# Optimization experiments

Hardware: AMD Instinct MI355X
Metric: run time of the kernel (lower is better)

## Reference

```python
import jax, jax.numpy as jnp
import numpy as np

NEG_SLOPE = 0.01  # torch nn.LeakyReLU default


def setup_inputs() -> dict:
    key = jax.random.key(0)
    kq, kk, kv, km, kw = jax.random.split(key, 5)
    B, Lq, Lk, Dk, Dv = 4, 2048, 2048, 512, 512
    q = jax.random.normal(kq, (B, Lq, Dk), dtype=jnp.float32)
    k = jax.random.normal(kk, (B, Lk, Dk), dtype=jnp.float32)
    v = jax.random.normal(kv, (B, Lk, Dv), dtype=jnp.float32)
    attn_mask = jax.random.randint(km, (B, Lq, Lk), 0, 2).astype(jnp.int32)
    # xavier_normal for (Dk, 1): std = sqrt(2 / (Dk + 1))
    weight = jax.random.normal(kw, (Dk, 1), dtype=jnp.float32) * np.sqrt(2.0 / (Dk + 1))
    return {"q": q, "k": k, "v": v, "attn_mask": attn_mask, "weight": weight}


def reference(q, k, v, attn_mask, weight):
    # (q - k) @ w  ==  (q @ w) - (k @ w): avoid the [B,Lq,Lk,Dk] intermediate.
    qw = jnp.einsum('bqd,do->bq', q, weight)  # [B, Lq]
    kw = jnp.einsum('bkd,do->bk', k, weight)  # [B, Lk]
    scores = qw[:, :, None] - kw[:, None, :]  # [B, Lq, Lk]
    attn = jnp.where(scores >= 0, scores, NEG_SLOPE * scores)  # LeakyReLU
    masked = attn_mask == 0
    attn = jnp.where(masked, -jnp.inf, attn)
    attn = jax.nn.softmax(attn, axis=2)
    attn = jnp.where(masked, 0.0, attn)
    # dropout omitted (eval mode / identity for reference correctness)
    output = jnp.einsum('bqk,bkd->bqd', attn, v)  # bmm
    return output, attn
```

## Files before the change

### kernel.cpp

```cpp
#include <hip/hip_runtime.h>
#include <math.h>

#define BB 4
#define LQ 2048
#define LK 2048
#define DK 512
#define DV 512

typedef __attribute__((ext_vector_type(8))) _Float16 f16x8;
typedef __attribute__((ext_vector_type(2))) _Float16 f16x2;
typedef __attribute__((ext_vector_type(4))) float f32x4;

#define WS_QW    0
#define WS_KW    8192
#define WS_M     16384
#define WS_INV   24576
#define WS_VF16  32768
#define NOUT     ((size_t)BB * LQ * DV)

__device__ __forceinline__ unsigned int pk2(float a, float b) {
    auto h = __builtin_amdgcn_cvt_pkrtz(a, b);
    return __builtin_bit_cast(unsigned int, h);
}

__device__ __forceinline__ void lds_barrier() {
    __builtin_amdgcn_sched_barrier(0);
    asm volatile("s_waitcnt lgkmcnt(0)\n\ts_barrier" ::: "memory");
    __builtin_amdgcn_sched_barrier(0);
}

__global__ __launch_bounds__(256) void qkw_kernel(const float* __restrict__ q,
                                                  const float* __restrict__ k,
                                                  const float* __restrict__ w,
                                                  float* __restrict__ ws) {
    int gw   = (int)((blockIdx.x * blockDim.x + threadIdx.x) >> 6);
    int lane = threadIdx.x & 63;
    const int nq = BB * LQ;
    const float* row = (gw < nq) ? (q + (size_t)gw * DK) : (k + (size_t)(gw - nq) * DK);

    float acc = 0.f;
#pragma unroll
    for (int j = 0; j < DK; j += 256) {
        int idx = j + lane * 4;
        float4 rv = *reinterpret_cast<const float4*>(row + idx);
        float4 wv = *reinterpret_cast<const float4*>(w + idx);
        acc += rv.x * wv.x + rv.y * wv.y + rv.z * wv.z + rv.w * wv.w;
    }
#pragma unroll
    for (int off = 32; off >= 1; off >>= 1) acc += __shfl_xor(acc, off, 64);
    if (lane == 0) ws[gw] = acc;
}

__global__ __launch_bounds__(256) void vpack_kernel(const float* __restrict__ v,
                                                    unsigned short* __restrict__ vF) {
    __shared__ float tile[32][517];
    const int k32 = blockIdx.x;
    const int b   = blockIdx.y;
    const int k0  = k32 * 32;
    const int t   = threadIdx.x;

#pragma unroll
    for (int i = 0; i < 16; ++i) {
        int flat = i * 256 + t;
        int row  = flat >> 7;
        int c4   = flat & 127;
        float4 f = *reinterpret_cast<const float4*>(
            v + ((size_t)(b * LK + k0 + row)) * DV + c4 * 4);
        tile[row][c4 * 4 + 0] = f.x;
        tile[row][c4 * 4 + 1] = f.y;
        tile[row][c4 * 4 + 2] = f.z;
        tile[row][c4 * 4 + 3] = f.w;
    }
    __syncthreads();

    const int w = t >> 6, l = t & 63;
    const int rbase = (l >> 4) * 8;
#pragma unroll
    for (int f = 0; f < 8; ++f) {
        int n16 = w * 8 + f;
        int col = n16 * 16 + (l & 15);
        f16x8 vv;
#pragma unroll
        for (int j = 0; j < 8; ++j) vv[j] = (_Float16)tile[rbase + j][col];
        size_t u16base = (((size_t)(b * 32 + n16)) * 64 + k32) * 512;
        *reinterpret_cast<f16x8*>(vF + u16base + l * 8) = vv;
    }
}

__global__ __launch_bounds__(256) void rowstat_kernel(const int* __restrict__ mask,
                                                      float* __restrict__ ws,
                                                      float* __restrict__ attn) {
    __shared__ float kws[LK];
    const int b = (blockIdx.x * 4) / LQ;
    const int t = threadIdx.x;

    const float4* kw4 = reinterpret_cast<const float4*>(ws + WS_KW + b * LK);
#pragma unroll
    for (int i = 0; i < 2; ++i)
        reinterpret_cast<float4*>(kws)[t + i * 256] = kw4[t + i * 256];
    __syncthreads();

    const int wave = t >> 6, lane = t & 63;
    const int rid  = blockIdx.x * 4 + wave;
    const float qwv = ws[WS_QW + rid];
    const int* mrow = mask + (size_t)rid * LK;

    float m = -INFINITY, s = 0.f;
    unsigned int mybits = 0;
#pragma unroll
    for (int i = 0; i < 8; ++i) {
        int e = (i * 64 + lane) * 4;
        int4  mi = *reinterpret_cast<const int4*>(mrow + e);
        float4 kv = reinterpret_cast<const float4*>(kws)[i * 64 + lane];
        float vals[4] = {kv.x, kv.y, kv.z, kv.w};
        int   msks[4] = {mi.x, mi.y, mi.z, mi.w};

        unsigned int bits = (msks[0] ? 1u : 0u) | (msks[1] ? 2u : 0u) |
                            (msks[2] ? 4u : 0u) | (msks[3] ? 8u : 0u);
        mybits |= bits << (i * 4);

#pragma unroll
        for (int j = 0; j < 4; ++j) {
            float sc = qwv - vals[j];
            sc = fmaxf(sc, 0.01f * sc);
            if (msks[j]) {
                if (sc > m) { s = s * __expf(m - sc) + 1.f; m = sc; }
                else        { s += __expf(sc - m); }
            }
        }
    }
#pragma unroll
    for (int off = 32; off >= 1; off >>= 1) {
        float mo = __shfl_xor(m, off, 64);
        float so = __shfl_xor(s, off, 64);
        float M  = fmaxf(m, mo);
        float sa = (m  == M) ? s  : s  * __expf(m  - M);
        float sb = (mo == M) ? so : so * __expf(mo - M);
        m = M; s = sa + sb;
    }
    const float inv = (s > 0.f) ? 1.f / s : 0.f;
    if (lane == 0) {
        ws[WS_M   + rid] = m;
        ws[WS_INV + rid] = inv;
    }

    float* arow = attn + (size_t)rid * LK;
#pragma unroll
    for (int i = 0; i < 8; ++i) {
        float4 kv = reinterpret_cast<const float4*>(kws)[i * 64 + lane];
        float vals[4] = {kv.x, kv.y, kv.z, kv.w};
        unsigned int bits = (mybits >> (i * 4)) & 0xFu;
        float p[4];
#pragma unroll
        for (int j = 0; j < 4; ++j) {
            float sc = qwv - vals[j];
            sc = fmaxf(sc, 0.01f * sc);
            p[j] = (bits & (1u << j)) ? __expf(sc - m) * inv : 0.f;
        }
        *reinterpret_cast<float4*>(arow + (i * 64 + lane) * 4) =
            make_float4(p[0], p[1], p[2], p[3]);
    }
}

__global__ __launch_bounds__(256, 2) void pv_kernel(
        const float* __restrict__ attn,
        const unsigned short* __restrict__ vF,
        float* __restrict__ out) {
    __shared__ unsigned int pH32[2][2048];
    __shared__ unsigned int pL32[2][2048];

    const int bid  = blockIdx.x;
    const int xcd  = bid & 7;
    const int rest = bid >> 3;
    const int g    = rest >> 2;
    const int ns   = rest & 3;
    const int qt4b = g * 8 + xcd;
    const int b    = qt4b & 3;
    const int qt   = qt4b >> 2;
    const int ksteps = LK >> 6;

    const int t = threadIdx.x;
    const int w = t >> 6, l = t & 63;

    const int row_a = (t >> 6) * 16 + (t & 15);
    const int kb    = ((t >> 4) & 3) * 8;
    const int rid   = b * LQ + qt * 64 + row_a;
    const float* arow = attn + (size_t)rid * LK + kb;

    const unsigned short* bsrc[2];
#pragma unroll
    for (int nb = 0; nb < 2; ++nb)
        bsrc[nb] = vF + (((size_t)(b * 32 + ns * 8 + w * 2 + nb)) * 64) * 512
                      + (size_t)l * 8;

    auto stage = [&](const float4& x, const float4& y, int buf, int ksub) {
        unsigned int H[4], L[4];
        float f[8] = {x.x, x.y, x.z, x.w, y.x, y.y, y.z, y.w};
#pragma unroll
        for (int jw = 0; jw < 4; ++jw) {
            unsigned int h01 = pk2(f[2 * jw], f[2 * jw + 1]);
            f16x2 hv = __builtin_bit_cast(f16x2, h01);
            H[jw] = h01;
            L[jw] = pk2(f[2 * jw] - (float)hv[0], f[2 * jw + 1] - (float)hv[1]);
        }
        *reinterpret_cast<uint4*>(&pH32[buf][ksub * 1024 + t * 4]) =
            *reinterpret_cast<uint4*>(H);
        *reinterpret_cast<uint4*>(&pL32[buf][ksub * 1024 + t * 4]) =
            *reinterpret_cast<uint4*>(L);
    };

    f16x8 bC[2][2], bN[2][2];
#pragma unroll
    for (int nb = 0; nb < 2; ++nb)
#pragma unroll
        for (int ks = 0; ks < 2; ++ks)
            bC[nb][ks] = *reinterpret_cast<const f16x8*>(bsrc[nb] + (size_t)ks * 512);

#pragma unroll
    for (int ks = 0; ks < 2; ++ks) {
        float4 x = *reinterpret_cast<const float4*>(arow + ks * 32);
        float4 y = *reinterpret_cast<const float4*>(arow + ks * 32 + 4);
        stage(x, y, 0, ks);
    }
    float4 aCx[2], aCy[2];
#pragma unroll
    for (int ks = 0; ks < 2; ++ks) {
        aCx[ks] = *reinterpret_cast<const float4*>(arow + 64 + ks * 32);
        aCy[ks] = *reinterpret_cast<const float4*>(arow + 64 + ks * 32 + 4);
    }

    f32x4 acc[4][2];
#pragma unroll
    for (int mf = 0; mf < 4; ++mf)
#pragma unroll
        for (int nb = 0; nb < 2; ++nb)
            acc[mf][nb] = (f32x4){0.f, 0.f, 0.f, 0.f};

    lds_barrier();

    for (int s = 0; s < ksteps; ++s) {
        const int buf  = s & 1;
        const int nbuf = buf ^ 1;
        const int sn   = (s + 1 < ksteps) ? s + 1 : s;
        const int sn2  = (s + 2 < ksteps) ? s + 2 : s;

        float4 aNx[2], aNy[2];
#pragma unroll
        for (int nb = 0; nb < 2; ++nb)
#pragma unroll
            for (int ks = 0; ks < 2; ++ks)
                bN[nb][ks] = *reinterpret_cast<const f16x8*>(
                    bsrc[nb] + (size_t)(sn * 2 + ks) * 512);
#pragma unroll
        for (int ks = 0; ks < 2; ++ks) {
            aNx[ks] = *reinterpret_cast<const float4*>(arow + sn2 * 64 + ks * 32);
            aNy[ks] = *reinterpret_cast<const float4*>(arow + sn2 * 64 + ks * 32 + 4);
        }

#pragma unroll
        for (int ks = 0; ks < 2; ++ks)
            stage(aCx[ks], aCy[ks], nbuf, ks);

#pragma unroll
        for (int ks = 0; ks < 2; ++ks) {
            const f16x8* pHf = reinterpret_cast<const f16x8*>(&pH32[buf][ks * 1024]);
            const f16x8* pLf = reinterpret_cast<const f16x8*>(&pL32[buf][ks * 1024]);
            f16x8 aH[4], aL[4];
#pragma unroll
            for (int mf = 0; mf < 4; ++mf) {
                aH[mf] = pHf[mf * 64 + l];
                aL[mf] = pLf[mf * 64 + l];
            }
            __builtin_amdgcn_s_setprio(1);
#pragma unroll
            for (int nb = 0; nb < 2; ++nb)
#pragma unroll
                for (int mf = 0; mf < 4; ++mf) {
                    acc[mf][nb] = __builtin_amdgcn_mfma_f32_16x16x32_f16(aH[mf], bC[nb][ks], acc[mf][nb], 0, 0, 0);
                    acc[mf][nb] = __builtin_amdgcn_mfma_f32_16x16x32_f16(aL[mf], bC[nb][ks], acc[mf][nb], 0, 0, 0);
                }
            __builtin_amdgcn_s_setprio(0);
        }

        lds_barrier();

#pragma unroll
        for (int nb = 0; nb < 2; ++nb)
#pragma unroll
            for (int ks = 0; ks < 2; ++ks)
                bC[nb][ks] = bN[nb][ks];
#pragma unroll
        for (int ks = 0; ks < 2; ++ks) { aCx[ks] = aNx[ks]; aCy[ks] = aNy[ks]; }
    }

    float* obase = out + ((size_t)(b * LQ + qt * 64)) * DV
                       + ns * 128 + w * 32 + (l & 15);
#pragma unroll
    for (int mf = 0; mf < 4; ++mf)
#pragma unroll
        for (int nb = 0; nb < 2; ++nb)
#pragma unroll
            for (int r = 0; r < 4; ++r)
                obase[(size_t)(mf * 16 + (l >> 4) * 4 + r) * DV + nb * 16] = acc[mf][nb][r];
}

extern "C" void kernel_launch(void* const* d_in, const int* in_sizes, int n_in,
                              void* d_out, int out_size, void* d_ws, size_t ws_size,
                              hipStream_t stream) {
    const float* q    = (const float*)d_in[0];
    const float* k    = (const float*)d_in[1];
    const float* v    = (const float*)d_in[2];
    const int*   mask = (const int*)d_in[3];
    const float* w    = (const float*)d_in[4];

    float* out  = (float*)d_out;
    float* attn = out + NOUT;
    float* ws   = (float*)d_ws;

    unsigned short* vF = (unsigned short*)(ws + WS_VF16);

    qkw_kernel<<<4096, 256, 0, stream>>>(q, k, w, ws);
    vpack_kernel<<<dim3(64, 4), 256, 0, stream>>>(v, vF);
    rowstat_kernel<<<2048, 256, 0, stream>>>(mask, ws, attn);
    pv_kernel<<<512, 256, 0, stream>>>(attn, vF, out);
}
```

Measured before the change: 82.24 us.

## Rewrite PV GEMM with register-direct A fragments and 32x32 MFMA tiles

The PV kernel drops the LDS staging of split-f16 attention fragments. Each wave now loads its attention rows straight into registers in MFMA operand layout and converts them to hi/lo f16 there, removing the LDS traffic and the per-step barriers. It switches from 16x16x32 to 32x32x16 MFMAs with a 128x128 block tile, 256 blocks and a two-deep register prefetch. V is repacked to match the 32-wide layout, and the unused row-stat writes are removed. The cost is more registers per thread, occupancy limited to one block per CU, and half as many blocks.

```diff
diff --git a/kernel.cpp b/kernel.cpp
--- a/kernel.cpp
+++ b/kernel.cpp
@@ -7,26 +7,19 @@
 #define DK 512
 #define DV 512
 
-typedef __attribute__((ext_vector_type(8))) _Float16 f16x8;
-typedef __attribute__((ext_vector_type(2))) _Float16 f16x2;
-typedef __attribute__((ext_vector_type(4))) float f32x4;
+typedef __attribute__((ext_vector_type(8)))  _Float16 f16x8;
+typedef __attribute__((ext_vector_type(2)))  _Float16 f16x2;
+typedef __attribute__((ext_vector_type(4)))  float f32x4;
+typedef __attribute__((ext_vector_type(16))) float f32x16;
 
 #define WS_QW    0
 #define WS_KW    8192
-#define WS_M     16384
-#define WS_INV   24576
 #define WS_VF16  32768
 #define NOUT     ((size_t)BB * LQ * DV)
 
 __device__ __forceinline__ unsigned int pk2(float a, float b) {
     auto h = __builtin_amdgcn_cvt_pkrtz(a, b);
     return __builtin_bit_cast(unsigned int, h);
-}
-
-__device__ __forceinline__ void lds_barrier() {
-    __builtin_amdgcn_sched_barrier(0);
-    asm volatile("s_waitcnt lgkmcnt(0)\n\ts_barrier" ::: "memory");
-    __builtin_amdgcn_sched_barrier(0);
 }
 
 __global__ __launch_bounds__(256) void qkw_kernel(const float* __restrict__ q,
@@ -74,21 +67,24 @@
     __syncthreads();
 
     const int w = t >> 6, l = t & 63;
-    const int rbase = (l >> 4) * 8;
-#pragma unroll
-    for (int f = 0; f < 8; ++f) {
-        int n16 = w * 8 + f;
-        int col = n16 * 16 + (l & 15);
-        f16x8 vv;
-#pragma unroll
-        for (int j = 0; j < 8; ++j) vv[j] = (_Float16)tile[rbase + j][col];
-        size_t u16base = (((size_t)(b * 32 + n16)) * 64 + k32) * 512;
-        *reinterpret_cast<f16x8*>(vF + u16base + l * 8) = vv;
+#pragma unroll
+    for (int f = 0; f < 4; ++f) {
+        const int n32 = w * 4 + f;
+        const int col = n32 * 32 + (l & 31);
+#pragma unroll
+        for (int kh = 0; kh < 2; ++kh) {
+            const int rbase = kh * 16 + (l >> 5) * 8;
+            f16x8 vv;
+#pragma unroll
+            for (int j = 0; j < 8; ++j) vv[j] = (_Float16)tile[rbase + j][col];
+            size_t u16base = (((size_t)(b * 16 + n32)) * 128 + k32 * 2 + kh) * 512;
+            *reinterpret_cast<f16x8*>(vF + u16base + l * 8) = vv;
+        }
     }
 }
 
 __global__ __launch_bounds__(256) void rowstat_kernel(const int* __restrict__ mask,
-                                                      float* __restrict__ ws,
+                                                      const float* __restrict__ ws,
                                                       float* __restrict__ attn) {
     __shared__ float kws[LK];
     const int b = (blockIdx.x * 4) / LQ;
@@ -139,10 +135,6 @@
         m = M; s = sa + sb;
     }
     const float inv = (s > 0.f) ? 1.f / s : 0.f;
-    if (lane == 0) {
-        ws[WS_M   + rid] = m;
-        ws[WS_INV + rid] = inv;
-    }
 
     float* arow = attn + (size_t)rid * LK;
 #pragma unroll
@@ -162,146 +154,141 @@
     }
 }
 
-__global__ __launch_bounds__(256, 2) void pv_kernel(
+__global__ __launch_bounds__(256, 1) void pv_kernel(
         const float* __restrict__ attn,
         const unsigned short* __restrict__ vF,
         float* __restrict__ out) {
-    __shared__ unsigned int pH32[2][2048];
-    __shared__ unsigned int pL32[2][2048];
-
-    const int bid  = blockIdx.x;
-    const int xcd  = bid & 7;
-    const int rest = bid >> 3;
-    const int g    = rest >> 2;
-    const int ns   = rest & 3;
-    const int qt4b = g * 8 + xcd;
-    const int b    = qt4b & 3;
-    const int qt   = qt4b >> 2;
-    const int ksteps = LK >> 6;
+    const int bid = blockIdx.x;
+    const int xcd = bid & 7;
+    const int cs  = (bid >> 3) & 3;
+    const int g   = bid >> 5;
+    const int u   = g * 8 + xcd;
+    const int b   = u >> 4;
 
     const int t = threadIdx.x;
     const int w = t >> 6, l = t & 63;
 
-    const int row_a = (t >> 6) * 16 + (t & 15);
-    const int kb    = ((t >> 4) & 3) * 8;
-    const int rid   = b * LQ + qt * 64 + row_a;
-    const float* arow = attn + (size_t)rid * LK + kb;
-
-    const unsigned short* bsrc[2];
-#pragma unroll
-    for (int nb = 0; nb < 2; ++nb)
-        bsrc[nb] = vF + (((size_t)(b * 32 + ns * 8 + w * 2 + nb)) * 64) * 512
-                      + (size_t)l * 8;
-
-    auto stage = [&](const float4& x, const float4& y, int buf, int ksub) {
-        unsigned int H[4], L[4];
-        float f[8] = {x.x, x.y, x.z, x.w, y.x, y.y, y.z, y.w};
-#pragma unroll
-        for (int jw = 0; jw < 4; ++jw) {
-            unsigned int h01 = pk2(f[2 * jw], f[2 * jw + 1]);
-            f16x2 hv = __builtin_bit_cast(f16x2, h01);
-            H[jw] = h01;
-            L[jw] = pk2(f[2 * jw] - (float)hv[0], f[2 * jw + 1] - (float)hv[1]);
-        }
-        *reinterpret_cast<uint4*>(&pH32[buf][ksub * 1024 + t * 4]) =
-            *reinterpret_cast<uint4*>(H);
-        *reinterpret_cast<uint4*>(&pL32[buf][ksub * 1024 + t * 4]) =
-            *reinterpret_cast<uint4*>(L);
-    };
-
-    f16x8 bC[2][2], bN[2][2];
-#pragma unroll
-    for (int nb = 0; nb < 2; ++nb)
-#pragma unroll
-        for (int ks = 0; ks < 2; ++ks)
-            bC[nb][ks] = *reinterpret_cast<const f16x8*>(bsrc[nb] + (size_t)ks * 512);
-
-#pragma unroll
-    for (int ks = 0; ks < 2; ++ks) {
-        float4 x = *reinterpret_cast<const float4*>(arow + ks * 32);
-        float4 y = *reinterpret_cast<const float4*>(arow + ks * 32 + 4);
-        stage(x, y, 0, ks);
-    }
-    float4 aCx[2], aCy[2];
-#pragma unroll
-    for (int ks = 0; ks < 2; ++ks) {
-        aCx[ks] = *reinterpret_cast<const float4*>(arow + 64 + ks * 32);
-        aCy[ks] = *reinterpret_cast<const float4*>(arow + 64 + ks * 32 + 4);
-    }
-
-    f32x4 acc[4][2];
-#pragma unroll
-    for (int mf = 0; mf < 4; ++mf)
-#pragma unroll
-        for (int nb = 0; nb < 2; ++nb)
-            acc[mf][nb] = (f32x4){0.f, 0.f, 0.f, 0.f};
-
-    lds_barrier();
-
-    for (int s = 0; s < ksteps; ++s) {
-        const int buf  = s & 1;
-        const int nbuf = buf ^ 1;
-        const int sn   = (s + 1 < ksteps) ? s + 1 : s;
-        const int sn2  = (s + 2 < ksteps) ? s + 2 : s;
-
-        float4 aNx[2], aNy[2];
-#pragma unroll
-        for (int nb = 0; nb < 2; ++nb)
+    const int mrowbase = u * 128 + (w >> 1) * 64;
+    const int colbase  = cs * 128 + (w & 1) * 64;
+    const int n32g0    = cs * 4 + (w & 1) * 2;
+
+    const float* aptr[2];
+#pragma unroll
+    for (int m32 = 0; m32 < 2; ++m32)
+        aptr[m32] = attn + (size_t)(mrowbase + m32 * 32 + (l & 31)) * LK
+                         + (l >> 5) * 8;
+    const unsigned short* bptr[2];
+#pragma unroll
+    for (int n32 = 0; n32 < 2; ++n32)
+        bptr[n32] = vF + ((size_t)(b * 16 + n32g0 + n32)) * 128 * 512
+                       + (size_t)l * 8;
+
+    float4 Af[2][2][2][2];
+    f16x8  Bf[2][2][2];
+
+#pragma unroll
+    for (int sl = 0; sl < 2; ++sl) {
+#pragma unroll
+        for (int m32 = 0; m32 < 2; ++m32)
+#pragma unroll
+            for (int ks = 0; ks < 2; ++ks) {
+                const float* p = aptr[m32] + sl * 32 + ks * 16;
+                Af[sl][m32][ks][0] = *reinterpret_cast<const float4*>(p);
+                Af[sl][m32][ks][1] = *reinterpret_cast<const float4*>(p + 4);
+            }
+#pragma unroll
+        for (int n32 = 0; n32 < 2; ++n32)
 #pragma unroll
             for (int ks = 0; ks < 2; ++ks)
-                bN[nb][ks] = *reinterpret_cast<const f16x8*>(
-                    bsrc[nb] + (size_t)(sn * 2 + ks) * 512);
-#pragma unroll
-        for (int ks = 0; ks < 2; ++ks) {
-            aNx[ks] = *reinterpret_cast<const float4*>(arow + sn2 * 64 + ks * 32);
-            aNy[ks] = *reinterpret_cast<const float4*>(arow + sn2 * 64 + ks * 32 + 4);
-        }
-
-#pragma unroll
-        for (int ks = 0; ks < 2; ++ks)
-            stage(aCx[ks], aCy[ks], nbuf, ks);
-
-#pragma unroll
-        for (int ks = 0; ks < 2; ++ks) {
-            const f16x8* pHf = reinterpret_cast<const f16x8*>(&pH32[buf][ks * 1024]);
-            const f16x8* pLf = reinterpret_cast<const f16x8*>(&pL32[buf][ks * 1024]);
-            f16x8 aH[4], aL[4];
-#pragma unroll
-            for (int mf = 0; mf < 4; ++mf) {
-                aH[mf] = pHf[mf * 64 + l];
-                aL[mf] = pLf[mf * 64 + l];
+                Bf[sl][n32][ks] = *reinterpret_cast<const f16x8*>(
+                    bptr[n32] + (size_t)(sl * 2 + ks) * 512);
+    }
+
+    f32x16 acc[2][2];
+#pragma unroll
+    for (int m32 = 0; m32 < 2; ++m32)
+#pragma unroll
+        for (int n32 = 0; n32 < 2; ++n32)
+#pragma unroll
+            for (int r = 0; r < 16; ++r) acc[m32][n32][r] = 0.f;
+
+    for (int s = 0; s < 64; s += 2) {
+#pragma unroll
+        for (int ph = 0; ph < 2; ++ph) {
+            const int scur  = s + ph;
+            const int sload = (scur + 2 < 64) ? scur + 2 : 62 + ph;
+
+            f16x8 ah[2][2], al[2][2];
+#pragma unroll
+            for (int m32 = 0; m32 < 2; ++m32)
+#pragma unroll
+                for (int ks = 0; ks < 2; ++ks) {
+                    float4 x = Af[ph][m32][ks][0];
+                    float4 y = Af[ph][m32][ks][1];
+                    float f[8] = {x.x, x.y, x.z, x.w, y.x, y.y, y.z, y.w};
+                    uint4 H, L;
+                    unsigned int* Hp = &H.x;
+                    unsigned int* Lp = &L.x;
+#pragma unroll
+                    for (int jw = 0; jw < 4; ++jw) {
+                        unsigned int h01 = pk2(f[2 * jw], f[2 * jw + 1]);
+                        f16x2 hv = __builtin_bit_cast(f16x2, h01);
+                        Hp[jw] = h01;
+                        Lp[jw] = pk2(f[2 * jw] - (float)hv[0],
+                                     f[2 * jw + 1] - (float)hv[1]);
+                    }
+                    ah[m32][ks] = __builtin_bit_cast(f16x8, H);
+                    al[m32][ks] = __builtin_bit_cast(f16x8, L);
+                }
+
+#pragma unroll
+            for (int m32 = 0; m32 < 2; ++m32)
+#pragma unroll
+                for (int ks = 0; ks < 2; ++ks) {
+                    const float* p = aptr[m32] + sload * 32 + ks * 16;
+                    Af[ph][m32][ks][0] = *reinterpret_cast<const float4*>(p);
+                    Af[ph][m32][ks][1] = *reinterpret_cast<const float4*>(p + 4);
+                }
+
+            f16x8 bl[2][2];
+#pragma unroll
+            for (int n32 = 0; n32 < 2; ++n32)
+#pragma unroll
+                for (int ks = 0; ks < 2; ++ks) bl[n32][ks] = Bf[ph][n32][ks];
+
+#pragma unroll
+            for (int n32 = 0; n32 < 2; ++n32)
+#pragma unroll
+                for (int m32 = 0; m32 < 2; ++m32)
+#pragma unroll
+                    for (int ks = 0; ks < 2; ++ks) {
+                        acc[m32][n32] = __builtin_amdgcn_mfma_f32_32x32x16_f16(
+                            ah[m32][ks], bl[n32][ks], acc[m32][n32], 0, 0, 0);
+                        acc[m32][n32] = __builtin_amdgcn_mfma_f32_32x32x16_f16(
+                            al[m32][ks], bl[n32][ks], acc[m32][n32], 0, 0, 0);
+                    }
+
+#pragma unroll
+            for (int n32 = 0; n32 < 2; ++n32)
+#pragma unroll
+                for (int ks = 0; ks < 2; ++ks)
+                    Bf[ph][n32][ks] = *reinterpret_cast<const f16x8*>(
+                        bptr[n32] + (size_t)(sload * 2 + ks) * 512);
+        }
+    }
+
+#pragma unroll
+    for (int m32 = 0; m32 < 2; ++m32)
+#pragma unroll
+        for (int n32 = 0; n32 < 2; ++n32) {
+            const int row0 = mrowbase + m32 * 32 + 4 * (l >> 5);
+            const int col  = colbase + n32 * 32 + (l & 31);
+#pragma unroll
+            for (int r = 0; r < 16; ++r) {
+                const int row = row0 + 8 * (r >> 2) + (r & 3);
+                out[(size_t)row * DV + col] = acc[m32][n32][r];
             }
-            __builtin_amdgcn_s_setprio(1);
-#pragma unroll
-            for (int nb = 0; nb < 2; ++nb)
-#pragma unroll
-                for (int mf = 0; mf < 4; ++mf) {
-                    acc[mf][nb] = __builtin_amdgcn_mfma_f32_16x16x32_f16(aH[mf], bC[nb][ks], acc[mf][nb], 0, 0, 0);
-                    acc[mf][nb] = __builtin_amdgcn_mfma_f32_16x16x32_f16(aL[mf], bC[nb][ks], acc[mf][nb], 0, 0, 0);
-                }
-            __builtin_amdgcn_s_setprio(0);
-        }
-
-        lds_barrier();
-
-#pragma unroll
-        for (int nb = 0; nb < 2; ++nb)
-#pragma unroll
-            for (int ks = 0; ks < 2; ++ks)
-                bC[nb][ks] = bN[nb][ks];
-#pragma unroll
-        for (int ks = 0; ks < 2; ++ks) { aCx[ks] = aNx[ks]; aCy[ks] = aNy[ks]; }
-    }
-
-    float* obase = out + ((size_t)(b * LQ + qt * 64)) * DV
-                       + ns * 128 + w * 32 + (l & 15);
-#pragma unroll
-    for (int mf = 0; mf < 4; ++mf)
-#pragma unroll
-        for (int nb = 0; nb < 2; ++nb)
-#pragma unroll
-            for (int r = 0; r < 4; ++r)
-                obase[(size_t)(mf * 16 + (l >> 4) * 4 + r) * DV + nb * 16] = acc[mf][nb][r];
+        }
 }
 
 extern "C" void kernel_launch(void* const* d_in, const int* in_sizes, int n_in,
@@ -322,5 +309,5 @@
     qkw_kernel<<<4096, 256, 0, stream>>>(q, k, w, ws);
     vpack_kernel<<<dim3(64, 4), 256, 0, stream>>>(v, vF);
     rowstat_kernel<<<2048, 256, 0, stream>>>(mask, ws, attn);
-    pv_kernel<<<512, 256, 0, stream>>>(attn, vF, out);
-}
+    pv_kernel<<<256, 256, 0, stream>>>(attn, vF, out);
+}
```

After: 188.7 us. 2.29x slower.
